# Kernel tuning notes

Hardware: AMD Instinct MI355X
Metric: run time of the kernel (lower is better)

## Reference

```python
import jax, jax.numpy as jnp
import numpy as np

N_NODES = 50000
N_EDGES = 600000
DIM = 128
N_REL = 3
LN_EPS = 1e-5


def setup_inputs() -> dict:
    key = jax.random.key(0)
    ks = jax.random.split(key, 8)
    x = jax.random.normal(ks[0], (N_NODES, DIM), dtype=jnp.float32)
    edge_index = jax.random.randint(ks[1], (2, N_EDGES), 0, N_NODES, dtype=jnp.int64)
    edge_type = jax.random.randint(ks[2], (N_EDGES,), 0, N_REL, dtype=jnp.int64)
    # learned params
    relation_weights = jax.random.normal(ks[3], (N_REL, DIM, DIM), dtype=jnp.float32)
    lim = 1.0 / np.sqrt(DIM)
    lin_w = jax.random.uniform(ks[4], (DIM, DIM), dtype=jnp.float32, minval=-lim, maxval=lim)
    lin_b = jax.random.uniform(ks[5], (DIM,), dtype=jnp.float32, minval=-lim, maxval=lim)
    ln_gamma = jnp.ones((DIM,), dtype=jnp.float32)
    ln_beta = jnp.zeros((DIM,), dtype=jnp.float32)
    return {"x": x, "edge_index": edge_index, "edge_type": edge_type,
            "relation_weights": relation_weights, "lin_w": lin_w, "lin_b": lin_b,
            "ln_gamma": ln_gamma, "ln_beta": ln_beta}


def reference(x, edge_index, edge_type, relation_weights, lin_w, lin_b, ln_gamma, ln_beta):
    # x: [N, D]; edge_index: [2, E]; edge_type: [E]
    N = x.shape[0]
    src, dst = edge_index[0], edge_index[1]
    xs = x[src]  # gather: [E, D]
    # relation-wise masked GEMM accumulated into per-edge messages
    msg = jnp.zeros_like(xs)
    for r in range(relation_weights.shape[0]):  # small fixed relation loop
        mask = (edge_type == r)[:, None]
        msg = msg + jnp.where(mask, xs @ relation_weights[r], jnp.zeros((), x.dtype))
    agg = jax.ops.segment_sum(msg, dst, num_segments=N)  # scatter-add: [N, D]
    deg = jax.ops.segment_sum(jnp.ones_like(dst, dtype=x.dtype), dst, num_segments=N)
    deg = jnp.maximum(deg, 1.0)
    out = agg / deg[:, None]
    # linear + residual + LayerNorm (eps 1e-5, biased variance)
    h = x @ lin_w.T + lin_b + out
    mu = jnp.mean(h, axis=-1, keepdims=True)
    var = jnp.mean((h - mu) ** 2, axis=-1, keepdims=True)
    return ln_gamma * (h - mu) * jax.lax.rsqrt(var + LN_EPS) + ln_beta
```

## Files before the change

kernel.cpp:

```cpp
#include <hip/hip_runtime.h>

#define DIM    128
#define NREL   3
#define KS     (NREL*DIM)
#define NB     16
#define LN_EPS 1e-5f
#define PPART  96
#define KSLOT  8
#define PW     (PPART*KSLOT)
#define OVFCAP 16384
#define CH     256
#define GPREP  352

typedef unsigned int uint;
typedef unsigned char uchar;
typedef float f32x4 __attribute__((ext_vector_type(4)));
typedef short short8 __attribute__((ext_vector_type(8)));

__device__ __forceinline__ unsigned short f2bf(float f) {
    union { float f; uint u; } c; c.f = f;
    return (unsigned short)((c.u + 0x7fffu + ((c.u >> 16) & 1u)) >> 16);
}
__device__ __forceinline__ uint packbf(float a, float b) {
    return (uint)f2bf(a) | ((uint)f2bf(b) << 16);
}
__device__ __forceinline__ float blo(uint u) {
    union { uint u; float f; } c; c.u = u << 16; return c.f;
}
__device__ __forceinline__ float bhi(uint u) {
    union { uint u; float f; } c; c.u = u & 0xffff0000u; return c.f;
}
__device__ __forceinline__ int ldidx(const int* p, size_t i, int i64) {
    return i64 ? p[2*i] : p[i];
}
__device__ __forceinline__ int fo(int m, int k) {
    return ((k >> 5) << 6) + ((((k >> 3) & 3)) << 4) + m;
}
__device__ __forceinline__ int SW(int s) { return s ^ ((s >> 4) & 7); }

__device__ __forceinline__ void block_probe(const int* __restrict__ ei, int t, int* s_i64) {
    if (t < 64) {
        int z = 0;
        #pragma unroll
        for (int i = 0; i < 4; i++) z += (ei[t*4 + i] == 0) ? 1 : 0;
        #pragma unroll
        for (int off = 1; off < 64; off <<= 1) z += __shfl_xor(z, off);
        if (t == 0) *s_i64 = (z > 64) ? 1 : 0;
    }
}

__device__ __forceinline__ void bpack_work(int idx, const float* __restrict__ relw,
                                           const float* __restrict__ linw,
                                           unsigned short* __restrict__ Bpack) {
    if (idx < 8192) {
        int lane = idx & 63, kk = (idx >> 6) & 15, tile = idx >> 10;
        int q = lane >> 4, n = tile * 16 + (lane & 15);
        uint vv[4];
        #pragma unroll
        for (int jp = 0; jp < 4; jp++) {
            int k0 = kk * 32 + q * 8 + jp * 2;
            float v0 = (k0     < KS) ? relw[(size_t)k0*DIM + n]
                                     : linw[(size_t)n*DIM + (k0 - KS)];
            float v1 = (k0 + 1 < KS) ? relw[(size_t)(k0+1)*DIM + n]
                                     : linw[(size_t)n*DIM + (k0 + 1 - KS)];
            vv[jp] = packbf(v0, v1);
        }
        uint4 v; v.x = vv[0]; v.y = vv[1]; v.z = vv[2]; v.w = vv[3];
        ((uint4*)Bpack)[idx] = v;
    }
}

__global__ __launch_bounds__(256)
void prep_kernel(const int* __restrict__ ei, const int* __restrict__ et,
                 const float* __restrict__ x, int E, int N, int Ee, int NBIN,
                 uchar* __restrict__ cnt, int* __restrict__ binbuf,
                 int* __restrict__ ovf_cnt, int2* __restrict__ ovf,
                 const float* __restrict__ relw, const float* __restrict__ linw,
                 unsigned short* __restrict__ Bpack, unsigned short* __restrict__ xbf)
{
    extern __shared__ int lhist[];
    __shared__ int s_i64;
    const int b = blockIdx.x, t = threadIdx.x;

    if (b < PPART) {
        block_probe(ei, t, &s_i64);
        for (int i = t; i < NBIN; i += 256) lhist[i] = 0;
        __syncthreads();
        const int i64 = s_i64;
        const int e0 = b * Ee;
        const int e1 = min(E, e0 + Ee);
        for (int e = e0 + t; e < e1; e += 256) {
            int s = ldidx(ei, (size_t)e, i64);
            int d = ldidx(ei, (size_t)E + e, i64);
            int r = ldidx(et, (size_t)e, i64);
            int bin = d >> 4;
            int tag = s | ((d & 15) << 20) | (r << 24);
            int lr = atomicAdd(&lhist[bin], 1);
            if (lr < KSLOT) {
                binbuf[bin * PW + b * KSLOT + lr] = tag;
            } else {
                int oi = atomicAdd(ovf_cnt, 1);
                if (oi < OVFCAP) ovf[oi] = make_int2(tag, bin);
            }
        }
        __syncthreads();
        for (int i = t; i < NBIN; i += 256)
            cnt[i * PPART + b] = (uchar)min(lhist[i], KSLOT);
    } else {
        const int cb = b - PPART;
        const int nconv = GPREP - PPART;
        const float4* x4 = (const float4*)x;
        const int items = N * (DIM / 8);
        for (int i = cb * 256 + t; i < items; i += nconv * 256) {
            float4 a = x4[i*2], bb = x4[i*2 + 1];
            uint4 v;
            v.x = packbf(a.x, a.y); v.y = packbf(a.z, a.w);
            v.z = packbf(bb.x, bb.y); v.w = packbf(bb.z, bb.w);
            ((uint4*)xbf)[i] = v;
        }
        bpack_work(cb * 256 + t, relw, linw, Bpack);
    }
}

__global__ __launch_bounds__(256)
void main_kernel(const unsigned short* __restrict__ xbf,
                 const uchar* __restrict__ cnt,
                 const int* __restrict__ binbuf,
                 const int* __restrict__ ovf_cnt, const int2* __restrict__ ovf,
                 const unsigned short* __restrict__ Bpack,
                 const float* __restrict__ linb,
                 const float* __restrict__ gamma,
                 const float* __restrict__ beta,
                 float* __restrict__ out, int N)
{
    __shared__ uint4 Af[1024];
    __shared__ int s_tag[CH];
    __shared__ int s_cmp[CH];
    __shared__ int s_map[CH];
    __shared__ int s_cnt[48];
    __shared__ int s_off[49];
    __shared__ int s_cur[48];
    __shared__ int s_coff[PPART + 1];
    __shared__ int s_n;
    __shared__ float s_mu[NB], s_rs[NB];

    const int t  = threadIdx.x;
    const int bb = blockIdx.x;
    const int n0 = bb * NB;
    const int m  = t >> 4;
    const int c  = t & 15;
    const int n  = n0 + m;

    const uint4* xh = (const uint4*)xbf;

    float a0[8], a1[8], a2[8];
    #pragma unroll
    for (int i = 0; i < 8; i++) { a0[i] = 0.f; a1[i] = 0.f; a2[i] = 0.f; }
    int deg = 0;
    uint4 res = {0,0,0,0};
    if (n < N) res = xh[(size_t)n*16 + c];

    if (t < PPART) s_coff[t + 1] = (int)cnt[(size_t)bb * PPART + t];
    if (t == 0) s_coff[0] = 0;
    __syncthreads();
    for (int off = 1; off < PPART; off <<= 1) {
        int v = 0;
        if (t < PPART) { v = s_coff[t + 1]; if (t >= off) v += s_coff[t + 1 - off]; }
        __syncthreads();
        if (t < PPART) s_coff[t + 1] = v;
        __syncthreads();
    }

    #define FINISH_CHUNK(NC) { \
        const int nc_ = (NC); \
        if (t < 64) { \
            int cv_ = (t < 48) ? s_cnt[t] : 0; \
            int v_ = cv_; \
            _Pragma("unroll") \
            for (int off = 1; off < 64; off <<= 1) { \
                int u_ = __shfl_up(v_, off); \
                if (t >= off) v_ += u_; \
            } \
            if (t < 48) { s_off[t + 1] = v_; s_cur[t] = v_ - cv_; } \
            if (t == 0) s_off[0] = 0; \
        } \
        __syncthreads(); \
        if (t < nc_) { \
            int pos_ = atomicAdd(&s_cur[key], 1); \
            s_cmp[pos_] = tg & 0xFFFFF; \
        } \
        __syncthreads(); \
        deg += s_off[m*3 + 3] - s_off[m*3]; \
        { \
            int p_ = s_off[m*3 + 0], pe_ = s_off[m*3 + 1]; \
            GATH(a0) \
            p_ = s_off[m*3 + 1]; pe_ = s_off[m*3 + 2]; \
            GATH(a1) \
            p_ = s_off[m*3 + 2]; pe_ = s_off[m*3 + 3]; \
            GATH(a2) \
        } \
        __syncthreads(); }

    #define GATH(ACC) \
        for (; p_ + 3 < pe_; p_ += 4) { \
            int s0 = s_cmp[p_],   s1 = s_cmp[p_+1]; \
            int s2 = s_cmp[p_+2], s3 = s_cmp[p_+3]; \
            uint4 g0 = xh[(size_t)s0*16 + c], g1 = xh[(size_t)s1*16 + c]; \
            uint4 g2 = xh[(size_t)s2*16 + c], g3 = xh[(size_t)s3*16 + c]; \
            ACC[0] += blo(g0.x)+blo(g1.x)+blo(g2.x)+blo(g3.x); \
            ACC[1] += bhi(g0.x)+bhi(g1.x)+bhi(g2.x)+bhi(g3.x); \
            ACC[2] += blo(g0.y)+blo(g1.y)+blo(g2.y)+blo(g3.y); \
            ACC[3] += bhi(g0.y)+bhi(g1.y)+bhi(g2.y)+bhi(g3.y); \
            ACC[4] += blo(g0.z)+blo(g1.z)+blo(g2.z)+blo(g3.z); \
            ACC[5] += bhi(g0.z)+bhi(g1.z)+bhi(g2.z)+bhi(g3.z); \
            ACC[6] += blo(g0.w)+blo(g1.w)+blo(g2.w)+blo(g3.w); \
            ACC[7] += bhi(g0.w)+bhi(g1.w)+bhi(g2.w)+bhi(g3.w); \
        } \
        for (; p_ < pe_; ++p_) { \
            int s0 = s_cmp[p_]; \
            uint4 g0 = xh[(size_t)s0*16 + c]; \
            ACC[0] += blo(g0.x); ACC[1] += bhi(g0.x); \
            ACC[2] += blo(g0.y); ACC[3] += bhi(g0.y); \
            ACC[4] += blo(g0.z); ACC[5] += bhi(g0.z); \
            ACC[6] += blo(g0.w); ACC[7] += bhi(g0.w); \
        }

    int g0 = 0;
    while (g0 < PPART) {
        const int base0 = s_coff[g0];
        int gend = g0;
        while (gend < PPART && s_coff[gend + 1] - base0 <= CH) ++gend;
        const int nc = s_coff[gend] - base0;
        if (t < 48) s_cnt[t] = 0;
        for (int cell = g0 + t; cell < gend; cell += 256) {
            int lo = s_coff[cell] - base0, hi = s_coff[cell + 1] - base0;
            for (int s2 = lo; s2 < hi; ++s2) s_map[s2] = cell;
        }
        __syncthreads();
        int key = -1, tg = 0;
        if (t < nc) {
            int cell = s_map[t];
            int slot = t - (s_coff[cell] - base0);
            tg = binbuf[(size_t)bb * PW + cell * KSLOT + slot];
            key = (((tg >> 20) & 15) * 3) + ((tg >> 24) & 3);
            atomicAdd(&s_cnt[key], 1);
        }
        __syncthreads();
        FINISH_CHUNK(nc)
        g0 = gend;
    }

    {
        int L = min(ovf_cnt[0], OVFCAP);
        if (L > 0) {
            if (t == 0) s_n = 0;
            if (t < 48) s_cnt[t] = 0;
            __syncthreads();
            for (int i = t; i < L; i += 256) {
                int2 o = ovf[i];
                if (o.y == bb) {
                    int pos = atomicAdd(&s_n, 1);
                    if (pos < CH) s_tag[pos] = o.x;
                }
            }
            __syncthreads();
            int nc = min(s_n, CH);
            int key = -1, tg = 0;
            if (t < nc) {
                tg = s_tag[t];
                key = (((tg >> 20) & 15) * 3) + ((tg >> 24) & 3);
                atomicAdd(&s_cnt[key], 1);
            }
            __syncthreads();
            FINISH_CHUNK(nc)
        }
    }
    #undef GATH
    #undef FINISH_CHUNK

    {
        float inv = 1.0f / fmaxf((float)deg, 1.0f);
        uint4 w0;
        w0.x = packbf(a0[0]*inv, a0[1]*inv); w0.y = packbf(a0[2]*inv, a0[3]*inv);
        w0.z = packbf(a0[4]*inv, a0[5]*inv); w0.w = packbf(a0[6]*inv, a0[7]*inv);
        Af[SW(fo(m, 0*DIM + 8*c))] = w0;
        w0.x = packbf(a1[0]*inv, a1[1]*inv); w0.y = packbf(a1[2]*inv, a1[3]*inv);
        w0.z = packbf(a1[4]*inv, a1[5]*inv); w0.w = packbf(a1[6]*inv, a1[7]*inv);
        Af[SW(fo(m, 1*DIM + 8*c))] = w0;
        w0.x = packbf(a2[0]*inv, a2[1]*inv); w0.y = packbf(a2[2]*inv, a2[3]*inv);
        w0.z = packbf(a2[4]*inv, a2[5]*inv); w0.w = packbf(a2[6]*inv, a2[7]*inv);
        Af[SW(fo(m, 2*DIM + 8*c))] = w0;
        Af[SW(fo(m, KS + 8*c))] = res;
    }
    __syncthreads();

    const int lane = t & 63;
    const int w    = t >> 6;
    const int mm   = lane & 15;
    const int q    = lane >> 4;
    f32x4 acc0 = {0,0,0,0}, acc1 = {0,0,0,0};
    {
        const short8* Aq = (const short8*)Af;
        const short8* Bq = (const short8*)Bpack;
        #pragma unroll
        for (int kk = 0; kk < 16; kk++) {
            short8 a  = Aq[SW(kk*64 + lane)];
            short8 b0 = Bq[((w*2 + 0)*16 + kk)*64 + lane];
            short8 b1 = Bq[((w*2 + 1)*16 + kk)*64 + lane];
            acc0 = __builtin_amdgcn_mfma_f32_16x16x32_bf16(a, b0, acc0, 0, 0, 0);
            acc1 = __builtin_amdgcn_mfma_f32_16x16x32_bf16(a, b1, acc1, 0, 0, 0);
        }
    }
    __syncthreads();

    float* H = (float*)Af;
    {
        int rb = q * 4;
        #pragma unroll
        for (int nt = 0; nt < 2; nt++) {
            int d = (w*2 + nt)*16 + mm;
            float lb = linb[d];
            f32x4 a = (nt == 0) ? acc0 : acc1;
            #pragma unroll
            for (int i = 0; i < 4; i++)
                H[(rb + i)*132 + d] = a[i] + lb;
        }
    }
    __syncthreads();

    {
        int j = t >> 4, p = t & 15;
        float s1 = 0.f, s2 = 0.f;
        const float* hr = &H[j*132 + p*8];
        #pragma unroll
        for (int i = 0; i < 8; i++) { float v = hr[i]; s1 += v; s2 += v*v; }
        #pragma unroll
        for (int off = 1; off < 16; off <<= 1) {
            s1 += __shfl_xor(s1, off);
            s2 += __shfl_xor(s2, off);
        }
        if (p == 0) {
            float mu  = s1 * (1.0f/DIM);
            float var = s2 * (1.0f/DIM) - mu*mu;
            s_mu[j] = mu;
            s_rs[j] = rsqrtf(var + LN_EPS);
        }
    }
    __syncthreads();

    {
        int d  = t & 127;
        int jb = (t >> 7) * 8;
        float g = gamma[d];
        float b = beta[d];
        #pragma unroll
        for (int jj = 0; jj < 8; jj++) {
            int j = jb + jj;
            int nn = n0 + j;
            if (nn < N) {
                float hv = H[j*132 + d];
                out[(size_t)nn*DIM + d] = g * (hv - s_mu[j]) * s_rs[j] + b;
            }
        }
    }
}

extern "C" void kernel_launch(void* const* d_in, const int* in_sizes, int n_in,
                              void* d_out, int out_size, void* d_ws, size_t ws_size,
                              hipStream_t stream)
{
    const float* x   = (const float*)d_in[0];
    const int*   ei  = (const int*)d_in[1];
    const int*   et  = (const int*)d_in[2];
    const float* rw  = (const float*)d_in[3];
    const float* lw  = (const float*)d_in[4];
    const float* lb  = (const float*)d_in[5];
    const float* lg  = (const float*)d_in[6];
    const float* lbe = (const float*)d_in[7];

    const int N    = in_sizes[0] / DIM;
    const int E    = in_sizes[2];
    const int NBIN = (N + NB - 1) / NB;
    const int Ee   = (E + PPART - 1) / PPART;

    char* wp = (char*)d_ws;
    int*  ovf_cnt = (int*)wp;             wp += 16;
    int2* ovf     = (int2*)wp;            wp += (size_t)OVFCAP * 8;
    uchar* cnt    = (uchar*)wp;           wp += ((size_t)NBIN * PPART + 63) & ~(size_t)63;
    int*  binbuf  = (int*)wp;             wp += (size_t)NBIN * PW * 4;
    unsigned short* Bpack = (unsigned short*)wp;   wp += 512 * 128 * 2;
    unsigned short* xbf   = (unsigned short*)wp;   wp += (size_t)N * DIM * 2;
    (void)ws_size;

    hipMemsetAsync(ovf_cnt, 0, 4, stream);
    prep_kernel<<<GPREP, 256, (size_t)NBIN * 4, stream>>>(ei, et, x, E, N, Ee, NBIN,
                                                          cnt, binbuf, ovf_cnt, ovf,
                                                          rw, lw, Bpack, xbf);
    main_kernel<<<NBIN, 256, 0, stream>>>(xbf, cnt, binbuf, ovf_cnt, ovf, Bpack,
                                          lb, lg, lbe, (float*)d_out, N);
}
```

Before: 192.5 us.

## Use fewer, larger binning partitions with per-partition overflow and drop memset

Binning now uses 32 partitions of 1024 threads with 24 slots per bin instead of 96 partitions with 8 slots. This shrinks the per-bin count scan, and the prefix over counts becomes a wavefront shuffle scan instead of a barrier loop. Overflow moves from a single global atomic counter to per-partition shared counters and buffers, which removes the memset launch. The main kernel aliases its tag scratch arrays onto the A tile in shared memory to cut LDS use. In exchange, the binbuf slot layout is larger per bin, and overflow lists are capped per partition.

```diff
diff --git a/kernel.cpp b/kernel.cpp
--- a/kernel.cpp
+++ b/kernel.cpp
@@ -5,12 +5,12 @@
 #define KS     (NREL*DIM)
 #define NB     16
 #define LN_EPS 1e-5f
-#define PPART  96
-#define KSLOT  8
+#define PPART  32
+#define KSLOT  24
 #define PW     (PPART*KSLOT)
-#define OVFCAP 16384
+#define OVFP   512
 #define CH     256
-#define GPREP  352
+#define GPREP  1024
 
 typedef unsigned int uint;
 typedef unsigned char uchar;
@@ -70,7 +70,7 @@
     }
 }
 
-__global__ __launch_bounds__(256)
+__global__ __launch_bounds__(1024)
 void prep_kernel(const int* __restrict__ ei, const int* __restrict__ et,
                  const float* __restrict__ x, int E, int N, int Ee, int NBIN,
                  uchar* __restrict__ cnt, int* __restrict__ binbuf,
@@ -80,16 +80,18 @@
 {
     extern __shared__ int lhist[];
     __shared__ int s_i64;
+    __shared__ int s_ovf;
     const int b = blockIdx.x, t = threadIdx.x;
 
     if (b < PPART) {
         block_probe(ei, t, &s_i64);
-        for (int i = t; i < NBIN; i += 256) lhist[i] = 0;
+        if (t == 0) s_ovf = 0;
+        for (int i = t; i < NBIN; i += 1024) lhist[i] = 0;
         __syncthreads();
         const int i64 = s_i64;
         const int e0 = b * Ee;
         const int e1 = min(E, e0 + Ee);
-        for (int e = e0 + t; e < e1; e += 256) {
+        for (int e = e0 + t; e < e1; e += 1024) {
             int s = ldidx(ei, (size_t)e, i64);
             int d = ldidx(ei, (size_t)E + e, i64);
             int r = ldidx(et, (size_t)e, i64);
@@ -99,26 +101,27 @@
             if (lr < KSLOT) {
                 binbuf[bin * PW + b * KSLOT + lr] = tag;
             } else {
-                int oi = atomicAdd(ovf_cnt, 1);
-                if (oi < OVFCAP) ovf[oi] = make_int2(tag, bin);
+                int oi = atomicAdd(&s_ovf, 1);
+                if (oi < OVFP) ovf[b * OVFP + oi] = make_int2(tag, bin);
             }
         }
         __syncthreads();
-        for (int i = t; i < NBIN; i += 256)
+        for (int i = t; i < NBIN; i += 1024)
             cnt[i * PPART + b] = (uchar)min(lhist[i], KSLOT);
+        if (t == 0) ovf_cnt[b] = min(s_ovf, OVFP);
     } else {
-        const int cb = b - PPART;
-        const int nconv = GPREP - PPART;
+        const int cid  = (b - PPART) * 1024 + t;
+        const int nthr = (GPREP - PPART) * 1024;
         const float4* x4 = (const float4*)x;
         const int items = N * (DIM / 8);
-        for (int i = cb * 256 + t; i < items; i += nconv * 256) {
+        for (int i = cid; i < items; i += nthr) {
             float4 a = x4[i*2], bb = x4[i*2 + 1];
             uint4 v;
             v.x = packbf(a.x, a.y); v.y = packbf(a.z, a.w);
             v.z = packbf(bb.x, bb.y); v.w = packbf(bb.z, bb.w);
             ((uint4*)xbf)[i] = v;
         }
-        bpack_work(cb * 256 + t, relw, linw, Bpack);
+        bpack_work(cid, relw, linw, Bpack);
     }
 }
 
@@ -134,15 +137,17 @@
                  float* __restrict__ out, int N)
 {
     __shared__ uint4 Af[1024];
-    __shared__ int s_tag[CH];
-    __shared__ int s_cmp[CH];
-    __shared__ int s_map[CH];
     __shared__ int s_cnt[48];
     __shared__ int s_off[49];
     __shared__ int s_cur[48];
     __shared__ int s_coff[PPART + 1];
     __shared__ int s_n;
+    __shared__ int s_ovfL;
     __shared__ float s_mu[NB], s_rs[NB];
+
+    int* s_tag = (int*)Af;
+    int* s_cmp = (int*)Af + 256;
+    int* s_map = (int*)Af + 512;
 
     const int t  = threadIdx.x;
     const int bb = blockIdx.x;
@@ -160,16 +165,24 @@
     uint4 res = {0,0,0,0};
     if (n < N) res = xh[(size_t)n*16 + c];
 
-    if (t < PPART) s_coff[t + 1] = (int)cnt[(size_t)bb * PPART + t];
-    if (t == 0) s_coff[0] = 0;
+    if (t < 64) {
+        int cv = (t < PPART) ? (int)cnt[(size_t)bb * PPART + t] : 0;
+        int v = cv;
+        #pragma unroll
+        for (int off = 1; off < PPART; off <<= 1) {
+            int u = __shfl_up(v, off);
+            if (t >= off) v += u;
+        }
+        if (t < PPART) s_coff[t + 1] = v;
+        if (t == 0) s_coff[0] = 0;
+    }
+    if (t >= 64 && t < 128) {
+        int lv = (t - 64 < PPART) ? ovf_cnt[t - 64] : 0;
+        #pragma unroll
+        for (int off = 1; off < 64; off <<= 1) lv += __shfl_xor(lv, off);
+        if (t == 64) s_ovfL = lv;
+    }
     __syncthreads();
-    for (int off = 1; off < PPART; off <<= 1) {
-        int v = 0;
-        if (t < PPART) { v = s_coff[t + 1]; if (t >= off) v += s_coff[t + 1 - off]; }
-        __syncthreads();
-        if (t < PPART) s_coff[t + 1] = v;
-        __syncthreads();
-    }
 
     #define FINISH_CHUNK(NC) { \
         const int nc_ = (NC); \
@@ -250,30 +263,30 @@
         g0 = gend;
     }
 
-    {
-        int L = min(ovf_cnt[0], OVFCAP);
-        if (L > 0) {
-            if (t == 0) s_n = 0;
-            if (t < 48) s_cnt[t] = 0;
-            __syncthreads();
+    if (s_ovfL > 0) {
+        if (t == 0) s_n = 0;
+        if (t < 48) s_cnt[t] = 0;
+        __syncthreads();
+        for (int p = 0; p < PPART; p++) {
+            int L = ovf_cnt[p];
             for (int i = t; i < L; i += 256) {
-                int2 o = ovf[i];
+                int2 o = ovf[p * OVFP + i];
                 if (o.y == bb) {
                     int pos = atomicAdd(&s_n, 1);
                     if (pos < CH) s_tag[pos] = o.x;
                 }
             }
-            __syncthreads();
-            int nc = min(s_n, CH);
-            int key = -1, tg = 0;
-            if (t < nc) {
-                tg = s_tag[t];
-                key = (((tg >> 20) & 15) * 3) + ((tg >> 24) & 3);
-                atomicAdd(&s_cnt[key], 1);
-            }
-            __syncthreads();
-            FINISH_CHUNK(nc)
-        }
+        }
+        __syncthreads();
+        int nc = min(s_n, CH);
+        int key = -1, tg = 0;
+        if (t < nc) {
+            tg = s_tag[t];
+            key = (((tg >> 20) & 15) * 3) + ((tg >> 24) & 3);
+            atomicAdd(&s_cnt[key], 1);
+        }
+        __syncthreads();
+        FINISH_CHUNK(nc)
     }
     #undef GATH
     #undef FINISH_CHUNK
@@ -384,18 +397,17 @@
     const int Ee   = (E + PPART - 1) / PPART;
 
     char* wp = (char*)d_ws;
-    int*  ovf_cnt = (int*)wp;             wp += 16;
-    int2* ovf     = (int2*)wp;            wp += (size_t)OVFCAP * 8;
+    int*  ovf_cnt = (int*)wp;             wp += 128;
+    int2* ovf     = (int2*)wp;            wp += (size_t)PPART * OVFP * 8;
     uchar* cnt    = (uchar*)wp;           wp += ((size_t)NBIN * PPART + 63) & ~(size_t)63;
     int*  binbuf  = (int*)wp;             wp += (size_t)NBIN * PW * 4;
     unsigned short* Bpack = (unsigned short*)wp;   wp += 512 * 128 * 2;
     unsigned short* xbf   = (unsigned short*)wp;   wp += (size_t)N * DIM * 2;
     (void)ws_size;
 
-    hipMemsetAsync(ovf_cnt, 0, 4, stream);
-    prep_kernel<<<GPREP, 256, (size_t)NBIN * 4, stream>>>(ei, et, x, E, N, Ee, NBIN,
-                                                          cnt, binbuf, ovf_cnt, ovf,
-                                                          rw, lw, Bpack, xbf);
+    prep_kernel<<<GPREP, 1024, (size_t)NBIN * 4, stream>>>(ei, et, x, E, N, Ee, NBIN,
+                                                           cnt, binbuf, ovf_cnt, ovf,
+                                                           rw, lw, Bpack, xbf);
     main_kernel<<<NBIN, 256, 0, stream>>>(xbf, cnt, binbuf, ovf_cnt, ovf, Bpack,
                                           lb, lg, lbe, (float*)d_out, N);
 }
```

Measured after the change: 188.0 us. 2.4% less time.
